# Kernel optimization log

Hardware: AMD Instinct MI355X
Metric: run time of the kernel (lower is better)

## Reference

```python
import jax, jax.numpy as jnp
import numpy as np

D_MODEL = 1024
N_HEADS = 16
HEAD_DIM = D_MODEL // N_HEADS


def setup_inputs() -> dict:
    key = jax.random.key(0)
    ks = jax.random.split(key, 5)
    B, T = 4, 2048
    scale = 0.02
    x = jax.random.normal(ks[0], (B, T, D_MODEL), dtype=jnp.float32)
    W_qkv = jax.random.normal(ks[1], (D_MODEL, 3 * D_MODEL), dtype=jnp.float32) * scale
    b_qkv = jnp.zeros((3 * D_MODEL,), dtype=jnp.float32)
    W_out = jax.random.normal(ks[2], (D_MODEL, D_MODEL), dtype=jnp.float32) * scale
    b_out = jnp.zeros((D_MODEL,), dtype=jnp.float32)
    return {"x": x, "W_qkv": W_qkv, "b_qkv": b_qkv, "W_out": W_out, "b_out": b_out}


def reference(x, W_qkv, b_qkv, W_out, b_out):
    B, T, C = x.shape
    H, Dh = N_HEADS, HEAD_DIM
    qkv = x @ W_qkv + b_qkv                      # (B,T,3C)
    q, k, v = jnp.split(qkv, 3, axis=-1)
    # (B,T,C) -> (B,H,T,Dh)
    q = q.reshape(B, T, H, Dh).transpose(0, 2, 1, 3)
    k = k.reshape(B, T, H, Dh).transpose(0, 2, 1, 3)
    v = v.reshape(B, T, H, Dh).transpose(0, 2, 1, 3)
    scores = jnp.einsum("bhqd,bhkd->bhqk", q, k) / jnp.sqrt(jnp.float32(Dh))
    causal = jnp.tril(jnp.ones((T, T), dtype=bool))  # True = keep
    scores = jnp.where(causal, scores, jnp.float32(-jnp.inf))
    attn = jax.nn.softmax(scores, axis=-1)
    out = jnp.einsum("bhqk,bhkd->bhqd", attn, v)  # (B,H,T,Dh)
    concat = out.transpose(0, 2, 1, 3).reshape(B, T, C)
    return concat @ W_out + b_out
```

## Files before the change

### kernel.cpp

```cpp
#include <hip/hip_runtime.h>
#include <math.h>

typedef __attribute__((ext_vector_type(8))) short bf16x8;
typedef __attribute__((ext_vector_type(4))) float f32x4;
typedef unsigned short u16;
typedef unsigned int u32;

#define TSEQ 2048
#define NH   16
#define DH   64
#define CDIM 1024
#define SCLQ 0.18033688011112042f

__device__ __forceinline__ u16 f2bf(float f) {
    union { float f; u32 u; } v; v.f = f;
    u32 r = v.u + 0x7fffu + ((v.u >> 16) & 1u);
    return (u16)(r >> 16);
}

__device__ __forceinline__ u32 cvtpk(float lo, float hi) {
    u32 r;
    asm("v_cvt_pk_bf16_f32 %0, %1, %2" : "=v"(r) : "v"(lo), "v"(hi));
    return r;
}

__device__ __forceinline__ float max3f(float a, float b, float c) {
    return fmaxf(fmaxf(a, b), c);
}

__device__ __forceinline__ void gl_lds16(const void* g, void* l) {
    __builtin_amdgcn_global_load_lds(
        (const __attribute__((address_space(1))) u32*)g,
        (__attribute__((address_space(3))) u32*)l, 16, 0, 0);
}

#define MFMA16(a, b, c) __builtin_amdgcn_mfma_f32_16x16x32_bf16(a, b, c, 0, 0, 0)

#define BAR()   do { __builtin_amdgcn_s_barrier(); __builtin_amdgcn_sched_barrier(0); } while (0)
#define WAITV(n) do { asm volatile("s_waitcnt vmcnt(" #n ")" ::: "memory"); \
                      __builtin_amdgcn_sched_barrier(0); } while (0)
#define WAITL() do { asm volatile("s_waitcnt lgkmcnt(0)" ::: "memory"); \
                     __builtin_amdgcn_sched_barrier(0); } while (0)

__global__ __launch_bounds__(256) void cvt_bf16(const float* __restrict__ in,
                                                u16* __restrict__ out, int n) {
    int i = (blockIdx.x * 256 + threadIdx.x) * 8;
    if (i >= n) return;
    float4 a = *(const float4*)(in + i);
    float4 b = *(const float4*)(in + i + 4);
    u16 o[8] = {f2bf(a.x), f2bf(a.y), f2bf(a.z), f2bf(a.w),
                f2bf(b.x), f2bf(b.y), f2bf(b.z), f2bf(b.w)};
    *(uint4*)(out + i) = *(const uint4*)o;
}

__global__ __launch_bounds__(256) void tr_w_bf16(const float* __restrict__ Wf,
                                                 u16* __restrict__ Wt, int K, int N) {
    __shared__ float tile[32][33];
    int n0 = blockIdx.x * 32, k0 = blockIdx.y * 32;
    int tx = threadIdx.x, ty = threadIdx.y;
#pragma unroll
    for (int r = 0; r < 4; r++)
        tile[ty + r * 8][tx] = Wf[(k0 + ty + r * 8) * N + n0 + tx];
    __syncthreads();
#pragma unroll
    for (int r = 0; r < 4; r++)
        Wt[(n0 + ty + r * 8) * K + k0 + tx] = f2bf(tile[tx][ty + r * 8]);
}

template <int EPI>
__global__ __launch_bounds__(512, 2) void gemm_8p(
    const u16* __restrict__ A, const u16* __restrict__ Bt,
    const float* __restrict__ bias,
    u16* __restrict__ O0, u16* __restrict__ O1, u16* __restrict__ O2,
    float* __restrict__ Of) {
    __shared__ u16 lA[2][128 * 64];
    __shared__ u16 lB[2][2][128 * 64];

    const int tid = threadIdx.x;
    const int lane = tid & 63, w = tid >> 6;
    const int l15 = lane & 15, l4 = lane >> 4;
    const int wm = w >> 2, wn = w & 3;

    const int nwg = gridDim.x, cpx = nwg >> 3;
    const int wg = (blockIdx.x & 7) * cpx + (blockIdx.x >> 3);
    const int mi = wg & 63, ni = wg >> 6;
    const int mb = mi * 128, nb = ni * 256;
    const int KD = 1024;

    auto stA = [&](int t, int p) {
        int kb = (t & 15) * 64;
#pragma unroll
        for (int s = 0; s < 2; s++) {
            int idx = s * 512 + tid;
            int row = idx >> 3, g = idx & 7;
            int gsw = g ^ (row & 7);
            gl_lds16(A + (size_t)(mb + row) * KD + kb + gsw * 8, &lA[p][idx * 8]);
        }
    };
    auto stB = [&](int t, int rb, int p) {
        int kb = (t & 15) * 64;
#pragma unroll
        for (int s = 0; s < 2; s++) {
            int idx = s * 512 + tid;
            int row = idx >> 3, g = idx & 7;
            int nrow = (row & 31) + ((row >> 5) << 6) + rb * 32;
            int gsw = g ^ (row & 7);
            gl_lds16(Bt + (size_t)(nb + nrow) * KD + kb + gsw * 8,
                     &lB[p][rb][idx * 8]);
        }
    };

    f32x4 zero = {0.f, 0.f, 0.f, 0.f};
    f32x4 acc[4][4];
#pragma unroll
    for (int i = 0; i < 4; i++)
#pragma unroll
        for (int j = 0; j < 4; j++) acc[i][j] = zero;

    const int sw = l15 & 7;
    const int aRow = wm * 64 + l15;
    const int bRow = wn * 32 + l15;
    const int g0 = (l4 ^ sw) * 8, g1 = ((4 + l4) ^ sw) * 8;

    stA(0, 0); stB(0, 0, 0); stB(0, 1, 0);
    stA(1, 1); stB(1, 0, 1);
    WAITV(4);
    BAR();

    bf16x8 af[4][2], b0[2][2], b1[2][2];

    for (int j = 0; j < 8; j++) {
#pragma unroll
        for (int fm = 0; fm < 4; fm++) {
            const u16* base = &lA[0][(aRow + fm * 16) * 64];
            af[fm][0] = *(const bf16x8*)(base + g0);
            af[fm][1] = *(const bf16x8*)(base + g1);
        }
#pragma unroll
        for (int fn = 0; fn < 2; fn++) {
            const u16* base = &lB[0][0][(bRow + fn * 16) * 64];
            b0[fn][0] = *(const bf16x8*)(base + g0);
            b0[fn][1] = *(const bf16x8*)(base + g1);
        }
        stB(2 * j + 1, 1, 1);
        BAR(); WAITL();
        __builtin_amdgcn_s_setprio(1);
#pragma unroll
        for (int fm = 0; fm < 4; fm++)
#pragma unroll
            for (int fn = 0; fn < 2; fn++) {
                acc[fm][fn] = MFMA16(af[fm][0], b0[fn][0], acc[fm][fn]);
                acc[fm][fn] = MFMA16(af[fm][1], b0[fn][1], acc[fm][fn]);
            }
        __builtin_amdgcn_s_setprio(0);
        BAR();
#pragma unroll
        for (int fn = 0; fn < 2; fn++) {
            const u16* base = &lB[0][1][(bRow + fn * 16) * 64];
            b1[fn][0] = *(const bf16x8*)(base + g0);
            b1[fn][1] = *(const bf16x8*)(base + g1);
        }
        stA(2 * j + 2, 0); stB(2 * j + 2, 0, 0);
        WAITV(4);
        BAR(); WAITL();
        __builtin_amdgcn_s_setprio(1);
#pragma unroll
        for (int fm = 0; fm < 4; fm++)
#pragma unroll
            for (int fn = 0; fn < 2; fn++) {
                acc[fm][fn + 2] = MFMA16(af[fm][0], b1[fn][0], acc[fm][fn + 2]);
                acc[fm][fn + 2] = MFMA16(af[fm][1], b1[fn][1], acc[fm][fn + 2]);
            }
        __builtin_amdgcn_s_setprio(0);
        BAR();
#pragma unroll
        for (int fm = 0; fm < 4; fm++) {
            const u16* base = &lA[1][(aRow + fm * 16) * 64];
            af[fm][0] = *(const bf16x8*)(base + g0);
            af[fm][1] = *(const bf16x8*)(base + g1);
        }
#pragma unroll
        for (int fn = 0; fn < 2; fn++) {
            const u16* base = &lB[1][0][(bRow + fn * 16) * 64];
            b0[fn][0] = *(const bf16x8*)(base + g0);
            b0[fn][1] = *(const bf16x8*)(base + g1);
        }
        stB(2 * j + 2, 1, 0);
        BAR(); WAITL();
        __builtin_amdgcn_s_setprio(1);
#pragma unroll
        for (int fm = 0; fm < 4; fm++)
#pragma unroll
            for (int fn = 0; fn < 2; fn++) {
                acc[fm][fn] = MFMA16(af[fm][0], b0[fn][0], acc[fm][fn]);
                acc[fm][fn] = MFMA16(af[fm][1], b0[fn][1], acc[fm][fn]);
            }
        __builtin_amdgcn_s_setprio(0);
        BAR();
#pragma unroll
        for (int fn = 0; fn < 2; fn++) {
            const u16* base = &lB[1][1][(bRow + fn * 16) * 64];
            b1[fn][0] = *(const bf16x8*)(base + g0);
            b1[fn][1] = *(const bf16x8*)(base + g1);
        }
        stA(2 * j + 3, 1); stB(2 * j + 3, 0, 1);
        WAITV(4);
        BAR(); WAITL();
        __builtin_amdgcn_s_setprio(1);
#pragma unroll
        for (int fm = 0; fm < 4; fm++)
#pragma unroll
            for (int fn = 0; fn < 2; fn++) {
                acc[fm][fn + 2] = MFMA16(af[fm][0], b1[fn][0], acc[fm][fn + 2]);
                acc[fm][fn + 2] = MFMA16(af[fm][1], b1[fn][1], acc[fm][fn + 2]);
            }
        __builtin_amdgcn_s_setprio(0);
        BAR();
    }
    asm volatile("s_waitcnt vmcnt(0)" ::: "memory");
    __builtin_amdgcn_sched_barrier(0);

#pragma unroll
    for (int fm = 0; fm < 4; fm++)
#pragma unroll
        for (int fn = 0; fn < 4; fn++) {
            int n = nb + wn * 64 + fn * 16 + l15;
            int m0 = mb + wm * 64 + fm * 16 + l4 * 4;
            float bz = bias[n];
            if (EPI == 0) {
#pragma unroll
                for (int i = 0; i < 4; i++)
                    Of[(size_t)(m0 + i) * CDIM + n] = acc[fm][fn][i] + bz;
            } else {
                int which = n >> 10, hh = (n >> 6) & 15, d = n & 63;
                int b = m0 >> 11, t0 = m0 & 2047;
                if (which == 0) {
#pragma unroll
                    for (int i = 0; i < 4; i++)
                        O0[((b * NH + hh) * TSEQ + t0 + i) * DH + d] =
                            f2bf((acc[fm][fn][i] + bz) * SCLQ);
                } else if (which == 1) {
#pragma unroll
                    for (int i = 0; i < 4; i++)
                        O1[((b * NH + hh) * TSEQ + t0 + i) * DH + d] =
                            f2bf(acc[fm][fn][i] + bz);
                } else {
                    u16 ov[4];
#pragma unroll
                    for (int i = 0; i < 4; i++) ov[i] = f2bf(acc[fm][fn][i] + bz);
                    *(uint2*)&O2[((b * NH + hh) * DH + d) * TSEQ + t0] =
                        *(const uint2*)ov;
                }
            }
        }
}

__global__ __launch_bounds__(256, 4) void attn_mfma(
    const u16* __restrict__ Q, const u16* __restrict__ K,
    const u16* __restrict__ Vt, u16* __restrict__ Oc) {
    __shared__ u16 Kl[2][4096];
    __shared__ u16 Vl[2][4096];
    __shared__ u16 Pl[4096];

    const int tid = threadIdx.x;
    const int lane = tid & 63, w = tid >> 6;
    const int l15 = lane & 15, l4 = lane >> 4;
    const int bh = blockIdx.x & 63;
    const int pair = blockIdx.x >> 6;
    const int qt0 = pair, qt1 = 31 - pair;
    const int NT = qt1 + 1;

    const u16* Qb = Q + bh * TSEQ * DH;
    const u16* Kb = K + bh * TSEQ * DH;
    const u16* Vb = Vt + bh * DH * TSEQ;

    auto STAGE = [&](int kt, int p) {
#pragma unroll
        for (int r = 0; r < 2; r++) {
            int idx = r * 256 + tid;
            int row = idx >> 3, h = idx & 7;
            int hs = h ^ (row & 7);
            gl_lds16(Kb + (kt * 64 + row) * DH + hs * 8, &Kl[p][idx * 8]);
            gl_lds16(Vb + row * TSEQ + kt * 64 + hs * 8, &Vl[p][idx * 8]);
        }
    };

    const int qrow0 = qt0 * 64 + w * 16 + l15;
    const int qrow1 = qt1 * 64 + w * 16 + l15;
    bf16x8 q0a, q0b, q1a, q1b;
    {
        const u16* qp = Qb + qrow0 * DH + l4 * 8;
        q0a = *(const bf16x8*)(qp);
        q0b = *(const bf16x8*)(qp + 32);
    }
    {
        const u16* qp = Qb + qrow1 * DH + l4 * 8;
        q1a = *(const bf16x8*)(qp);
        q1b = *(const bf16x8*)(qp + 32);
    }

    f32x4 zero = {0.f, 0.f, 0.f, 0.f};
    f32x4 o0[4], o1[4];
    float m0 = -INFINITY, l0 = 0.f, m1 = -INFINITY, l1 = 0.f;
#pragma unroll
    for (int i = 0; i < 4; i++) { o0[i] = zero; o1[i] = zero; }

    auto SMPV = [&](f32x4* s, float& m_r, float& l_r, f32x4* oacc,
                    int q_row, bool domask, int kt, int p) {
        if (domask) {
#pragma unroll
            for (int c = 0; c < 4; c++)
#pragma unroll
                for (int i = 0; i < 4; i++) {
                    int kg = kt * 64 + c * 16 + l4 * 4 + i;
                    if (kg > q_row) s[c][i] = -INFINITY;
                }
        }
        float a0 = max3f(s[0][0], s[0][1], s[0][2]);
        float a1 = max3f(s[0][3], s[1][0], s[1][1]);
        float a2 = max3f(s[1][2], s[1][3], s[2][0]);
        float a3 = max3f(s[2][1], s[2][2], s[2][3]);
        float a4 = max3f(s[3][0], s[3][1], s[3][2]);
        float mx = max3f(max3f(a0, a1, a2), fmaxf(a3, a4), s[3][3]);
        mx = fmaxf(mx, __shfl_xor(mx, 16));
        mx = fmaxf(mx, __shfl_xor(mx, 32));
        if (!__all(mx <= m_r)) {
            float mnew = fmaxf(m_r, mx);
            float corr = __builtin_amdgcn_exp2f(m_r - mnew);
            l_r *= corr;
            float cr[4];
#pragma unroll
            for (int r = 0; r < 4; r++) cr[r] = __shfl(corr, l4 * 4 + r);
#pragma unroll
            for (int dg = 0; dg < 4; dg++)
#pragma unroll
                for (int r = 0; r < 4; r++) oacc[dg][r] *= cr[r];
            m_r = mnew;
        }
        float pv[16];
#pragma unroll
        for (int c = 0; c < 4; c++)
#pragma unroll
            for (int i = 0; i < 4; i++)
                pv[c * 4 + i] = __builtin_amdgcn_exp2f(s[c][i] - m_r);
        float t0 = (pv[0] + pv[1]) + (pv[2] + pv[3]);
        float t1 = (pv[4] + pv[5]) + (pv[6] + pv[7]);
        float t2 = (pv[8] + pv[9]) + (pv[10] + pv[11]);
        float t3 = (pv[12] + pv[13]) + (pv[14] + pv[15]);
        float rs = (t0 + t1) + (t2 + t3);
        rs += __shfl_xor(rs, 16);
        rs += __shfl_xor(rs, 32);
        l_r += rs;

#pragma unroll
        for (int c = 0; c < 4; c++) {
            uint2 pr;
            pr.x = cvtpk(pv[c * 4 + 0], pv[c * 4 + 1]);
            pr.y = cvtpk(pv[c * 4 + 2], pv[c * 4 + 3]);
            int g = (c << 1) + (l4 >> 1);
            int gp = g ^ (l15 & 7);
            *(uint2*)&Pl[w * 1024 + l15 * 64 + gp * 8 + ((l4 & 1) << 2)] = pr;
        }

        __builtin_amdgcn_s_setprio(1);
#pragma unroll
        for (int kk = 0; kk < 2; kk++) {
            int grp = ((kk << 2) + l4) ^ (l15 & 7);
            bf16x8 pf = *(const bf16x8*)&Pl[w * 1024 + l15 * 64 + grp * 8];
#pragma unroll
            for (int dg = 0; dg < 4; dg++) {
                int drow = (dg << 4) + l15;
                bf16x8 vf = *(const bf16x8*)(&Vl[p][drow * 64 + grp * 8]);
                oacc[dg] = MFMA16(pf, vf, oacc[dg]);
            }
        }
        __builtin_amdgcn_s_setprio(0);
    };

    STAGE(0, 0);

    for (int kt = 0; kt < NT; kt++) {
        const int p = kt & 1;
        __syncthreads();
        if (kt + 1 < NT) {
            STAGE(kt + 1, p ^ 1);
            asm volatile("s_waitcnt vmcnt(4)" ::: "memory");
        } else {
            asm volatile("s_waitcnt vmcnt(0)" ::: "memory");
        }
        __syncthreads();

        const bool act0 = (kt <= qt0);

        f32x4 s1[4], s0[4];
        __builtin_amdgcn_s_setprio(1);
#pragma unroll
        for (int c = 0; c < 4; c++) {
            int trow = c * 16 + l15;
            int swz = l15 & 7;
            bf16x8 kf0 = *(const bf16x8*)(&Kl[p][trow * 64 + (l4 ^ swz) * 8]);
            bf16x8 kf1 = *(const bf16x8*)(&Kl[p][trow * 64 + ((4 + l4) ^ swz) * 8]);
            f32x4 a = zero;
            a = MFMA16(kf0, q1a, a);
            a = MFMA16(kf1, q1b, a);
            s1[c] = a;
            if (act0) {
                f32x4 b = zero;
                b = MFMA16(kf0, q0a, b);
                b = MFMA16(kf1, q0b, b);
                s0[c] = b;
            }
        }
        __builtin_amdgcn_s_setprio(0);

        SMPV(s1, m1, l1, o1, qrow1, kt == qt1, kt, p);
        if (act0) {
            asm volatile("s_waitcnt lgkmcnt(0)" ::: "memory");
            SMPV(s0, m0, l0, o0, qrow0, kt == qt0, kt, p);
        }
    }

    const int b = bh >> 4, hh = bh & 15;
    {
        float inv[4];
#pragma unroll
        for (int r = 0; r < 4; r++) inv[r] = 1.0f / __shfl(l0, l4 * 4 + r);
        int tb = qt0 * 64 + w * 16 + l4 * 4;
#pragma unroll
        for (int r = 0; r < 4; r++)
#pragma unroll
            for (int dg = 0; dg < 4; dg++)
                Oc[(b * TSEQ + tb + r) * CDIM + hh * DH + (dg << 4) + l15] =
                    f2bf(o0[dg][r] * inv[r]);
    }
    {
        float inv[4];
#pragma unroll
        for (int r = 0; r < 4; r++) inv[r] = 1.0f / __shfl(l1, l4 * 4 + r);
        int tb = qt1 * 64 + w * 16 + l4 * 4;
#pragma unroll
        for (int r = 0; r < 4; r++)
#pragma unroll
            for (int dg = 0; dg < 4; dg++)
                Oc[(b * TSEQ + tb + r) * CDIM + hh * DH + (dg << 4) + l15] =
                    f2bf(o1[dg][r] * inv[r]);
    }
}

extern "C" void kernel_launch(void* const* d_in, const int* in_sizes, int n_in,
                              void* d_out, int out_size, void* d_ws, size_t ws_size,
                              hipStream_t stream) {
    const float* x     = (const float*)d_in[0];
    const float* W_qkv = (const float*)d_in[1];
    const float* b_qkv = (const float*)d_in[2];
    const float* W_out = (const float*)d_in[3];
    const float* b_out = (const float*)d_in[4];
    float* out = (float*)d_out;

    u16* xb  = (u16*)d_ws;
    u16* Wqt = xb  + 8388608;
    u16* Wot = Wqt + 3145728;
    u16* Qw  = Wot + 1048576;
    u16* Kw  = Qw  + 8388608;
    u16* Vtw = Kw  + 8388608;
    u16* Ocw = Vtw + 8388608;

    cvt_bf16<<<4096, 256, 0, stream>>>(x, xb, 8388608);
    tr_w_bf16<<<dim3(96, 32), dim3(32, 8), 0, stream>>>(W_qkv, Wqt, 1024, 3072);
    tr_w_bf16<<<dim3(32, 32), dim3(32, 8), 0, stream>>>(W_out, Wot, 1024, 1024);
    gemm_8p<1><<<768, 512, 0, stream>>>(xb, Wqt, b_qkv, Qw, Kw, Vtw, nullptr);
    attn_mfma<<<1024, 256, 0, stream>>>(Qw, Kw, Vtw, Ocw);
    gemm_8p<0><<<256, 512, 0, stream>>>(Ocw, Wot, b_out, nullptr, nullptr, nullptr, out);
}
```

Before: 266.3 us.

## Enlarge GEMM tiles to 256x256 and fuse preprocessing kernels into one launch

The GEMM moves from 128x256 tiles to 256x256 tiles, with each wave computing a 128x64 sub-tile. A and B are each double-buffered in two halves, and the 8-phase schedule interleaves LDS reads with global-to-LDS prefetch. Larger tiles raise arithmetic intensity and reuse of operands loaded into LDS. The cost is 128 accumulator registers per lane, occupancy of one block per CU, and fewer workgroups: 384 for the QKV GEMM and only 128 for the output GEMM, which may underfill the 256 CUs. The x conversion and the two weight transposes are merged into a single prep kernel, which removes two launches.

Measured after the change: 289.3 us. 8.7% more time.

```diff
diff --git a/kernel.cpp b/kernel.cpp
--- a/kernel.cpp
+++ b/kernel.cpp
@@ -36,28 +36,36 @@
 
 #define MFMA16(a, b, c) __builtin_amdgcn_mfma_f32_16x16x32_bf16(a, b, c, 0, 0, 0)
 
-#define BAR()   do { __builtin_amdgcn_s_barrier(); __builtin_amdgcn_sched_barrier(0); } while (0)
-#define WAITV(n) do { asm volatile("s_waitcnt vmcnt(" #n ")" ::: "memory"); \
-                      __builtin_amdgcn_sched_barrier(0); } while (0)
-#define WAITL() do { asm volatile("s_waitcnt lgkmcnt(0)" ::: "memory"); \
-                     __builtin_amdgcn_sched_barrier(0); } while (0)
-
-__global__ __launch_bounds__(256) void cvt_bf16(const float* __restrict__ in,
-                                                u16* __restrict__ out, int n) {
-    int i = (blockIdx.x * 256 + threadIdx.x) * 8;
-    if (i >= n) return;
-    float4 a = *(const float4*)(in + i);
-    float4 b = *(const float4*)(in + i + 4);
-    u16 o[8] = {f2bf(a.x), f2bf(a.y), f2bf(a.z), f2bf(a.w),
-                f2bf(b.x), f2bf(b.y), f2bf(b.z), f2bf(b.w)};
-    *(uint4*)(out + i) = *(const uint4*)o;
-}
-
-__global__ __launch_bounds__(256) void tr_w_bf16(const float* __restrict__ Wf,
-                                                 u16* __restrict__ Wt, int K, int N) {
+#define WAITV(n) do { asm volatile("s_waitcnt vmcnt(" #n ")" ::: "memory"); } while (0)
+#define WAITL()  do { asm volatile("s_waitcnt lgkmcnt(0)" ::: "memory"); } while (0)
+#define BARC()   do { __builtin_amdgcn_s_barrier(); __builtin_amdgcn_sched_barrier(0); } while (0)
+
+__global__ __launch_bounds__(256) void prep(
+    const float* __restrict__ x, const float* __restrict__ Wq,
+    const float* __restrict__ Wo,
+    u16* __restrict__ xb, u16* __restrict__ Wqt, u16* __restrict__ Wot) {
+    const int bid = blockIdx.x, tid = threadIdx.x;
+    if (bid < 4096) {
+        int i = (bid * 256 + tid) * 8;
+        float4 a = *(const float4*)(x + i);
+        float4 b = *(const float4*)(x + i + 4);
+        u16 o[8] = {f2bf(a.x), f2bf(a.y), f2bf(a.z), f2bf(a.w),
+                    f2bf(b.x), f2bf(b.y), f2bf(b.z), f2bf(b.w)};
+        *(uint4*)(xb + i) = *(const uint4*)o;
+        return;
+    }
     __shared__ float tile[32][33];
-    int n0 = blockIdx.x * 32, k0 = blockIdx.y * 32;
-    int tx = threadIdx.x, ty = threadIdx.y;
+    const float* Wf; u16* Wt; int K, N, n0, k0;
+    if (bid < 4096 + 3072) {
+        int b2 = bid - 4096;
+        Wf = Wq; Wt = Wqt; K = 1024; N = 3072;
+        n0 = (b2 % 96) * 32; k0 = (b2 / 96) * 32;
+    } else {
+        int b2 = bid - 7168;
+        Wf = Wo; Wt = Wot; K = 1024; N = 1024;
+        n0 = (b2 & 31) * 32; k0 = (b2 >> 5) * 32;
+    }
+    int tx = tid & 31, ty = tid >> 5;
 #pragma unroll
     for (int r = 0; r < 4; r++)
         tile[ty + r * 8][tx] = Wf[(k0 + ty + r * 8) * N + n0 + tx];
@@ -68,164 +76,153 @@
 }
 
 template <int EPI>
-__global__ __launch_bounds__(512, 2) void gemm_8p(
+__global__ __launch_bounds__(512, 1) void gemm256(
     const u16* __restrict__ A, const u16* __restrict__ Bt,
     const float* __restrict__ bias,
     u16* __restrict__ O0, u16* __restrict__ O1, u16* __restrict__ O2,
     float* __restrict__ Of) {
-    __shared__ u16 lA[2][128 * 64];
+    __shared__ u16 lA[2][2][128 * 64];
     __shared__ u16 lB[2][2][128 * 64];
 
     const int tid = threadIdx.x;
     const int lane = tid & 63, w = tid >> 6;
     const int l15 = lane & 15, l4 = lane >> 4;
     const int wm = w >> 2, wn = w & 3;
-
-    const int nwg = gridDim.x, cpx = nwg >> 3;
-    const int wg = (blockIdx.x & 7) * cpx + (blockIdx.x >> 3);
-    const int mi = wg & 63, ni = wg >> 6;
-    const int mb = mi * 128, nb = ni * 256;
+    const int nwg = gridDim.x;
+    const int wg = (blockIdx.x & 7) * (nwg >> 3) + (blockIdx.x >> 3);
+    const int mi = wg & 31, ni = wg >> 5;
+    const size_t mb = (size_t)mi * 256, nb = (size_t)ni * 256;
     const int KD = 1024;
 
-    auto stA = [&](int t, int p) {
+    auto stA = [&](int t, int half, int buf) {
         int kb = (t & 15) * 64;
 #pragma unroll
         for (int s = 0; s < 2; s++) {
-            int idx = s * 512 + tid;
-            int row = idx >> 3, g = idx & 7;
+            int i2 = s * 512 + tid;
+            int row = i2 >> 3, g = i2 & 7;
             int gsw = g ^ (row & 7);
-            gl_lds16(A + (size_t)(mb + row) * KD + kb + gsw * 8, &lA[p][idx * 8]);
+            gl_lds16(A + (mb + half * 128 + row) * KD + kb + gsw * 8,
+                     &lA[buf][half][i2 * 8]);
         }
     };
-    auto stB = [&](int t, int rb, int p) {
+    auto stB = [&](int t, int half, int buf) {
         int kb = (t & 15) * 64;
 #pragma unroll
         for (int s = 0; s < 2; s++) {
-            int idx = s * 512 + tid;
-            int row = idx >> 3, g = idx & 7;
-            int nrow = (row & 31) + ((row >> 5) << 6) + rb * 32;
+            int i2 = s * 512 + tid;
+            int row = i2 >> 3, g = i2 & 7;
             int gsw = g ^ (row & 7);
-            gl_lds16(Bt + (size_t)(nb + nrow) * KD + kb + gsw * 8,
-                     &lB[p][rb][idx * 8]);
+            gl_lds16(Bt + (nb + half * 128 + row) * KD + kb + gsw * 8,
+                     &lB[buf][half][i2 * 8]);
         }
     };
 
     f32x4 zero = {0.f, 0.f, 0.f, 0.f};
-    f32x4 acc[4][4];
-#pragma unroll
-    for (int i = 0; i < 4; i++)
+    f32x4 acc[8][4];
+#pragma unroll
+    for (int i = 0; i < 8; i++)
 #pragma unroll
         for (int j = 0; j < 4; j++) acc[i][j] = zero;
 
-    const int sw = l15 & 7;
-    const int aRow = wm * 64 + l15;
-    const int bRow = wn * 32 + l15;
-    const int g0 = (l4 ^ sw) * 8, g1 = ((4 + l4) ^ sw) * 8;
-
-    stA(0, 0); stB(0, 0, 0); stB(0, 1, 0);
-    stA(1, 1); stB(1, 0, 1);
-    WAITV(4);
-    BAR();
-
-    bf16x8 af[4][2], b0[2][2], b1[2][2];
-
-    for (int j = 0; j < 8; j++) {
+    const int hB = wn >> 1, rBb = (wn & 1) * 64;
+
+    stB(0, 0, 0); stA(0, 0, 0); stB(0, 1, 0); stA(0, 1, 0);
+    stB(1, 0, 1); stA(1, 0, 1); stB(1, 1, 1);
+    WAITV(6);
+    BARC();
+
+    bf16x8 a8[4][2], bA[2][2], bB[2][2];
+
+    for (int t = 0; t < 16; t++) {
+        const int p = t & 1, q = p ^ 1;
 #pragma unroll
         for (int fm = 0; fm < 4; fm++) {
-            const u16* base = &lA[0][(aRow + fm * 16) * 64];
-            af[fm][0] = *(const bf16x8*)(base + g0);
-            af[fm][1] = *(const bf16x8*)(base + g1);
+            int r = fm * 16 + l15;
+            const u16* base = &lA[p][wm][r * 64];
+            a8[fm][0] = *(const bf16x8*)(base + ((l4) ^ (r & 7)) * 8);
+            a8[fm][1] = *(const bf16x8*)(base + ((4 + l4) ^ (r & 7)) * 8);
         }
 #pragma unroll
         for (int fn = 0; fn < 2; fn++) {
-            const u16* base = &lB[0][0][(bRow + fn * 16) * 64];
-            b0[fn][0] = *(const bf16x8*)(base + g0);
-            b0[fn][1] = *(const bf16x8*)(base + g1);
-        }
-        stB(2 * j + 1, 1, 1);
-        BAR(); WAITL();
+            int r = rBb + fn * 16 + l15;
+            const u16* base = &lB[p][hB][r * 64];
+            bA[fn][0] = *(const bf16x8*)(base + ((l4) ^ (r & 7)) * 8);
+            bA[fn][1] = *(const bf16x8*)(base + ((4 + l4) ^ (r & 7)) * 8);
+        }
+        stA(t + 1, 1, q);
+        __builtin_amdgcn_s_barrier();
+        WAITL();
         __builtin_amdgcn_s_setprio(1);
 #pragma unroll
         for (int fm = 0; fm < 4; fm++)
 #pragma unroll
             for (int fn = 0; fn < 2; fn++) {
-                acc[fm][fn] = MFMA16(af[fm][0], b0[fn][0], acc[fm][fn]);
-                acc[fm][fn] = MFMA16(af[fm][1], b0[fn][1], acc[fm][fn]);
-            }
-        __builtin_amdgcn_s_setprio(0);
-        BAR();
+                acc[fm][fn] = MFMA16(a8[fm][0], bA[fn][0], acc[fm][fn]);
+                acc[fm][fn] = MFMA16(a8[fm][1], bA[fn][1], acc[fm][fn]);
+            }
+        __builtin_amdgcn_s_setprio(0);
+        BARC();
 #pragma unroll
         for (int fn = 0; fn < 2; fn++) {
-            const u16* base = &lB[0][1][(bRow + fn * 16) * 64];
-            b1[fn][0] = *(const bf16x8*)(base + g0);
-            b1[fn][1] = *(const bf16x8*)(base + g1);
-        }
-        stA(2 * j + 2, 0); stB(2 * j + 2, 0, 0);
-        WAITV(4);
-        BAR(); WAITL();
+            int r = rBb + (fn + 2) * 16 + l15;
+            const u16* base = &lB[p][hB][r * 64];
+            bB[fn][0] = *(const bf16x8*)(base + ((l4) ^ (r & 7)) * 8);
+            bB[fn][1] = *(const bf16x8*)(base + ((4 + l4) ^ (r & 7)) * 8);
+        }
+        __builtin_amdgcn_s_barrier();
+        WAITL();
         __builtin_amdgcn_s_setprio(1);
 #pragma unroll
         for (int fm = 0; fm < 4; fm++)
 #pragma unroll
             for (int fn = 0; fn < 2; fn++) {
-                acc[fm][fn + 2] = MFMA16(af[fm][0], b1[fn][0], acc[fm][fn + 2]);
-                acc[fm][fn + 2] = MFMA16(af[fm][1], b1[fn][1], acc[fm][fn + 2]);
-            }
-        __builtin_amdgcn_s_setprio(0);
-        BAR();
+                acc[fm][fn + 2] = MFMA16(a8[fm][0], bB[fn][0], acc[fm][fn + 2]);
+                acc[fm][fn + 2] = MFMA16(a8[fm][1], bB[fn][1], acc[fm][fn + 2]);
+            }
+        __builtin_amdgcn_s_setprio(0);
+        BARC();
 #pragma unroll
         for (int fm = 0; fm < 4; fm++) {
-            const u16* base = &lA[1][(aRow + fm * 16) * 64];
-            af[fm][0] = *(const bf16x8*)(base + g0);
-            af[fm][1] = *(const bf16x8*)(base + g1);
-        }
-#pragma unroll
-        for (int fn = 0; fn < 2; fn++) {
-            const u16* base = &lB[1][0][(bRow + fn * 16) * 64];
-            b0[fn][0] = *(const bf16x8*)(base + g0);
-            b0[fn][1] = *(const bf16x8*)(base + g1);
-        }
-        stB(2 * j + 2, 1, 0);
-        BAR(); WAITL();
+            int r = (fm + 4) * 16 + l15;
+            const u16* base = &lA[p][wm][r * 64];
+            a8[fm][0] = *(const bf16x8*)(base + ((l4) ^ (r & 7)) * 8);
+            a8[fm][1] = *(const bf16x8*)(base + ((4 + l4) ^ (r & 7)) * 8);
+        }
+        stB(t + 2, 0, p);
+        __builtin_amdgcn_s_barrier();
+        WAITL();
         __builtin_amdgcn_s_setprio(1);
 #pragma unroll
         for (int fm = 0; fm < 4; fm++)
 #pragma unroll
             for (int fn = 0; fn < 2; fn++) {
-                acc[fm][fn] = MFMA16(af[fm][0], b0[fn][0], acc[fm][fn]);
-                acc[fm][fn] = MFMA16(af[fm][1], b0[fn][1], acc[fm][fn]);
-            }
-        __builtin_amdgcn_s_setprio(0);
-        BAR();
-#pragma unroll
-        for (int fn = 0; fn < 2; fn++) {
-            const u16* base = &lB[1][1][(bRow + fn * 16) * 64];
-            b1[fn][0] = *(const bf16x8*)(base + g0);
-            b1[fn][1] = *(const bf16x8*)(base + g1);
-        }
-        stA(2 * j + 3, 1); stB(2 * j + 3, 0, 1);
-        WAITV(4);
-        BAR(); WAITL();
+                acc[fm + 4][fn + 2] = MFMA16(a8[fm][0], bB[fn][0], acc[fm + 4][fn + 2]);
+                acc[fm + 4][fn + 2] = MFMA16(a8[fm][1], bB[fn][1], acc[fm + 4][fn + 2]);
+            }
+        __builtin_amdgcn_s_setprio(0);
+        BARC();
+        stA(t + 2, 0, p); stB(t + 2, 1, p);
+        __builtin_amdgcn_s_barrier();
         __builtin_amdgcn_s_setprio(1);
 #pragma unroll
         for (int fm = 0; fm < 4; fm++)
 #pragma unroll
             for (int fn = 0; fn < 2; fn++) {
-                acc[fm][fn + 2] = MFMA16(af[fm][0], b1[fn][0], acc[fm][fn + 2]);
-                acc[fm][fn + 2] = MFMA16(af[fm][1], b1[fn][1], acc[fm][fn + 2]);
-            }
-        __builtin_amdgcn_s_setprio(0);
-        BAR();
-    }
-    asm volatile("s_waitcnt vmcnt(0)" ::: "memory");
-    __builtin_amdgcn_sched_barrier(0);
-
-#pragma unroll
-    for (int fm = 0; fm < 4; fm++)
+                acc[fm + 4][fn] = MFMA16(a8[fm][0], bA[fn][0], acc[fm + 4][fn]);
+                acc[fm + 4][fn] = MFMA16(a8[fm][1], bA[fn][1], acc[fm + 4][fn]);
+            }
+        __builtin_amdgcn_s_setprio(0);
+        WAITV(6);
+        BARC();
+    }
+    WAITV(0);
+
+#pragma unroll
+    for (int fm = 0; fm < 8; fm++)
 #pragma unroll
         for (int fn = 0; fn < 4; fn++) {
-            int n = nb + wn * 64 + fn * 16 + l15;
-            int m0 = mb + wm * 64 + fm * 16 + l4 * 4;
+            int n = (int)nb + wn * 64 + fn * 16 + l15;
+            int m0 = (int)mb + wm * 128 + fm * 16 + l4 * 4;
             float bz = bias[n];
             if (EPI == 0) {
 #pragma unroll
@@ -465,10 +462,8 @@
     u16* Vtw = Kw  + 8388608;
     u16* Ocw = Vtw + 8388608;
 
-    cvt_bf16<<<4096, 256, 0, stream>>>(x, xb, 8388608);
-    tr_w_bf16<<<dim3(96, 32), dim3(32, 8), 0, stream>>>(W_qkv, Wqt, 1024, 3072);
-    tr_w_bf16<<<dim3(32, 32), dim3(32, 8), 0, stream>>>(W_out, Wot, 1024, 1024);
-    gemm_8p<1><<<768, 512, 0, stream>>>(xb, Wqt, b_qkv, Qw, Kw, Vtw, nullptr);
+    prep<<<8192, 256, 0, stream>>>(x, W_qkv, W_out, xb, Wqt, Wot);
+    gemm256<1><<<384, 512, 0, stream>>>(xb, Wqt, b_qkv, Qw, Kw, Vtw, nullptr);
     attn_mfma<<<1024, 256, 0, stream>>>(Qw, Kw, Vtw, Ocw);
-    gemm_8p<0><<<256, 512, 0, stream>>>(Ocw, Wot, b_out, nullptr, nullptr, nullptr, out);
-}
+    gemm256<0><<<128, 512, 0, stream>>>(Ocw, Wot, b_out, nullptr, nullptr, nullptr, out);
+}
```
